# Performance work log

Hardware: AMD Instinct MI355X
Metric: run time of the kernel (lower is better)

Reference implementation:

```python
import jax, jax.numpy as jnp
import numpy as np

BATCH = 2048
INPUT_DIM = 256    # == output_units, since Dense output is fed back into the cell
DEC_UNITS = 1024
OUTPUT_STEPS = 96
OUTPUT_UNITS = 256


def setup_inputs() -> dict:
    key = jax.random.key(0)
    ks = jax.random.split(key, 8)
    scale = 0.05
    return {
        "last_input": jax.random.normal(ks[0], (BATCH, INPUT_DIM), dtype=jnp.float32),
        "h0": jax.random.normal(ks[1], (BATCH, DEC_UNITS), dtype=jnp.float32),
        "c0": jax.random.normal(ks[2], (BATCH, DEC_UNITS), dtype=jnp.float32),
        # LSTMCell params (Keras layout: kernel [in, 4*units], recurrent_kernel [units, 4*units], bias [4*units]; gate order i,f,c,o)
        "Wk": jax.random.normal(ks[3], (INPUT_DIM, 4 * DEC_UNITS), dtype=jnp.float32) * scale,
        "Wr": jax.random.normal(ks[4], (DEC_UNITS, 4 * DEC_UNITS), dtype=jnp.float32) * scale,
        "b": jax.random.normal(ks[5], (4 * DEC_UNITS,), dtype=jnp.float32) * scale,
        # Dense output projection
        "Wd": jax.random.normal(ks[6], (DEC_UNITS, OUTPUT_UNITS), dtype=jnp.float32) * scale,
        "bd": jax.random.normal(ks[7], (OUTPUT_UNITS,), dtype=jnp.float32) * scale,
    }


def reference(last_input, h0, c0, Wk, Wr, b, Wd, bd):
    def step(carry, _):
        x, h, c = carry
        # fused gate GEMM: [B, in] @ [in, 4U] + [B, U] @ [U, 4U]
        z = x @ Wk + h @ Wr + b
        zi, zf, zg, zo = jnp.split(z, 4, axis=-1)  # Keras gate order: i, f, c(g), o
        i = jax.nn.sigmoid(zi)
        f = jax.nn.sigmoid(zf)
        o = jax.nn.sigmoid(zo)
        c_new = f * c + i * jnp.tanh(zg)
        h_new = o * jnp.tanh(c_new)
        pred = h_new @ Wd + bd  # fed back as next step's input
        return (pred, h_new, c_new), pred

    _, preds = jax.lax.scan(step, (last_input, h0, c0), None, length=OUTPUT_STEPS)
    # preds: [T, B, out] -> [B, T, out] (matches tf.transpose(predictions, [1,0,2]))
    return jnp.transpose(preds, (1, 0, 2))
```

## Files before the change

kernel.cpp:

```cpp
#include <hip/hip_runtime.h>
#include <hip/hip_bf16.h>
#include <stdint.h>

#define B_SZ 2048
#define U_SZ 1024
#define G_SZ 4096
#define I_SZ 256
#define O_SZ 256
#define T_SZ 96
#define K1_SZ 1280

typedef _Float16 half8 __attribute__((ext_vector_type(8)));
typedef float float4v __attribute__((ext_vector_type(4)));

__device__ inline float sigm_f(float x) { return 1.0f / (1.0f + __expf(-x)); }
__device__ inline float tanh_f(float x) { return 1.0f - 2.0f / (1.0f + __expf(2.0f * x)); }

__device__ inline short f2h(float x) {
    return __builtin_bit_cast(short, (_Float16)x);
}

__device__ inline void cp16(const void* g, void* l) {
    __builtin_amdgcn_global_load_lds(
        (const __attribute__((address_space(1))) void*)g,
        (__attribute__((address_space(3))) void*)l,
        16, 0, 0);
}


__global__ void transpose_reord(const float* __restrict__ in, float* __restrict__ out, int K) {
    __shared__ float s[32][33];
    int c0 = blockIdx.x * 32, k0 = blockIdx.y * 32;
    int tx = threadIdx.x, ty = threadIdx.y;
#pragma unroll
    for (int i = 0; i < 4; i++)
        s[ty + 8 * i][tx] = in[(long)(k0 + ty + 8 * i) * G_SZ + c0 + tx];
    __syncthreads();
#pragma unroll
    for (int i = 0; i < 4; i++) {
        int cc = ty + 8 * i;
        int c = c0 + cc;
        int n = 4 * (c & 1023) + (c >> 10);
        out[(long)n * K + k0 + tx] = s[tx][cc];
    }
}

__global__ void transpose_f32(const float* __restrict__ in, float* __restrict__ out, int R, int C) {
    __shared__ float s[32][33];
    int c0 = blockIdx.x * 32, r0 = blockIdx.y * 32;
    int tx = threadIdx.x, ty = threadIdx.y;
#pragma unroll
    for (int i = 0; i < 4; i++)
        s[ty + 8 * i][tx] = in[(long)(r0 + ty + 8 * i) * C + c0 + tx];
    __syncthreads();
#pragma unroll
    for (int i = 0; i < 4; i++)
        out[(long)(c0 + ty + 8 * i) * R + r0 + tx] = s[tx][ty + 8 * i];
}

__global__ void transpose_f16(const float* __restrict__ in, short* __restrict__ out, int R, int C) {
    __shared__ float s[32][33];
    int c0 = blockIdx.x * 32, r0 = blockIdx.y * 32;
    int tx = threadIdx.x, ty = threadIdx.y;
#pragma unroll
    for (int i = 0; i < 4; i++)
        s[ty + 8 * i][tx] = in[(long)(r0 + ty + 8 * i) * C + c0 + tx];
    __syncthreads();
#pragma unroll
    for (int i = 0; i < 4; i++)
        out[(long)(c0 + ty + 8 * i) * R + r0 + tx] = f2h(s[tx][ty + 8 * i]);
}

__global__ void fold_gemm(const float* __restrict__ WkT, const float* __restrict__ WrT,
                          const float* __restrict__ Wd, short* __restrict__ WeT) {
    __shared__ float sA[16][17];
    __shared__ float sB[16][17];
    int tx = threadIdx.x, ty = threadIdx.y;
    int n0 = blockIdx.x * 16, k0 = blockIdx.y * 16;
    float acc = 0.0f;
    for (int pc = 0; pc < I_SZ; pc += 16) {
        sA[ty][tx] = WkT[(long)(n0 + ty) * I_SZ + pc + tx];
        sB[ty][tx] = Wd[(long)(k0 + ty) * I_SZ + pc + tx];
        __syncthreads();
#pragma unroll
        for (int x = 0; x < 16; x++) acc += sA[ty][x] * sB[tx][x];
        __syncthreads();
    }
    long n = n0 + ty, k = k0 + tx;
    WeT[n * U_SZ + k] = f2h(WrT[n * U_SZ + k] + acc);
}

__global__ void build_b0t(const float* __restrict__ WkT, const float* __restrict__ WrT,
                          short* __restrict__ B0T) {
    long idx = (long)blockIdx.x * 256 + threadIdx.x;
    long n = idx / K1_SZ, k = idx % K1_SZ;
    float v = (k < I_SZ) ? WkT[n * I_SZ + k] : WrT[n * U_SZ + (k - I_SZ)];
    B0T[idx] = f2h(v);
}

__global__ void build_x0(const float* __restrict__ x0, const float* __restrict__ h0,
                         short* __restrict__ X0) {
    long idx = (long)blockIdx.x * 256 + threadIdx.x;
    long m = idx / K1_SZ, k = idx % K1_SZ;
    float v = (k < I_SZ) ? x0[m * I_SZ + k] : h0[m * U_SZ + (k - I_SZ)];
    X0[idx] = f2h(v);
}

__global__ void build_ber(const float* __restrict__ Wk, const float* __restrict__ b,
                          const float* __restrict__ bd, float* __restrict__ beR,
                          float* __restrict__ bR) {
    int c = blockIdx.x * 256 + threadIdx.x;
    float s = 0.0f;
    for (int p = 0; p < I_SZ; p++) s += bd[p] * Wk[(long)p * G_SZ + c];
    int slot = 4 * (c & 1023) + (c >> 10);
    bR[slot] = b[c];
    beR[slot] = b[c] + s;
}

__global__ __launch_bounds__(256, 2) void lstm_step(
    const short* __restrict__ A, const short* __restrict__ Bm, int K,
    float* __restrict__ cT, const float* __restrict__ beR, short* __restrict__ hOut) {
    __shared__ char smem[65536];

    const int tid = threadIdx.x;
    const int w = tid >> 6, l = tid & 63;
    const int wg = w >> 1, wb = w & 1;
    const int n_blk = blockIdx.x, m_blk = blockIdx.y;
    const long Kb = (long)K * 2;

    float4v acc[4][4];
#pragma unroll
    for (int i = 0; i < 4; i++)
#pragma unroll
        for (int j = 0; j < 4; j++) acc[i][j] = (float4v)0.0f;

    const int r8 = l >> 3;
    const int s8 = l & 7;
    const int gch = s8 ^ r8;
    const char* gA = (const char*)A + ((long)(n_blk * 128 + w * 32 + r8)) * Kb + gch * 16;
    const char* gB = (const char*)Bm + ((long)(m_blk * 128 + w * 32 + r8)) * Kb + gch * 16;

    const int lr = l & 15;
    const int lk = l >> 4;

    auto stage = [&](int kt, int b) {
        const long go = (long)kt * 128;
        char* lA = smem + b * 32768 + (w * 32) * 128;
        char* lB = smem + b * 32768 + 16384 + (w * 32) * 128;
#pragma unroll
        for (int ci = 0; ci < 4; ++ci) {
            cp16(gA + (long)ci * 8 * Kb + go, lA + ci * 1024);
            cp16(gB + (long)ci * 8 * Kb + go, lB + ci * 1024);
        }
    };
    auto compute = [&](int b) {
        const char* As = smem + b * 32768;
        const char* Bs = smem + b * 32768 + 16384;
#pragma unroll
        for (int ks = 0; ks < 2; ++ks) {
            half8 af[4], bf[4];
            const int chunk = (ks * 4 + lk) ^ (lr & 7);
#pragma unroll
            for (int mi = 0; mi < 4; ++mi)
                af[mi] = *(const half8*)(As + (wg * 64 + mi * 16 + lr) * 128 + chunk * 16);
#pragma unroll
            for (int ni = 0; ni < 4; ++ni)
                bf[ni] = *(const half8*)(Bs + (wb * 64 + ni * 16 + lr) * 128 + chunk * 16);
#pragma unroll
            for (int mi = 0; mi < 4; ++mi)
#pragma unroll
                for (int ni = 0; ni < 4; ++ni)
                    acc[mi][ni] = __builtin_amdgcn_mfma_f32_16x16x32_f16(
                        af[mi], bf[ni], acc[mi][ni], 0, 0, 0);
        }
    };

    const int KI = K >> 6;
    stage(0, 0);
    for (int kt = 0; kt < KI; kt += 2) {
        __syncthreads();
        if (kt + 1 < KI) stage(kt + 1, 1);
        compute(0);
        __syncthreads();
        if (kt + 2 < KI) stage(kt + 2, 0);
        compute(1);
    }

    short* hs = (short*)smem;
    __syncthreads();
    const int j_base = n_blk * 32 + wg * 16;
    const int m_base = m_blk * 128 + wb * 64;
#pragma unroll
    for (int mi = 0; mi < 4; ++mi) {
        int j = j_base + mi * 4 + lk;
        float4v bias = *(const float4v*)(beR + 4 * j);
#pragma unroll
        for (int ni = 0; ni < 4; ++ni) {
            int m = m_base + ni * 16 + lr;
            float zi = acc[mi][ni][0] + bias[0];
            float zf = acc[mi][ni][1] + bias[1];
            float zg = acc[mi][ni][2] + bias[2];
            float zo = acc[mi][ni][3] + bias[3];
            float ig = sigm_f(zi), fg = sigm_f(zf), gg = tanh_f(zg), og = sigm_f(zo);
            long cidx = (long)j * B_SZ + m;
            float cn = fg * cT[cidx] + ig * gg;
            cT[cidx] = cn;
            float h = og * tanh_f(cn);
            hs[(wb * 64 + ni * 16 + lr) * 32 + (wg * 16 + mi * 4 + lk)] = f2h(h);
        }
    }
    __syncthreads();
    {
        int q = tid & 3;
        for (int rr = tid >> 2; rr < 128; rr += 64) {
            uint4 v = *(const uint4*)(hs + rr * 32 + q * 8);
            *(uint4*)(hOut + (long)(m_blk * 128 + rr) * U_SZ + n_blk * 32 + q * 8) = v;
        }
    }
}

__global__ __launch_bounds__(256, 2) void dense_out(
    const short* __restrict__ Hm, const short* __restrict__ WdT,
    const float* __restrict__ bd, float* __restrict__ out, int t_fix) {
    __shared__ char smem[65536];

    const int tid = threadIdx.x;
    const int w = tid >> 6, l = tid & 63;
    const int wg = w >> 1, wb = w & 1;
    const int m_blk = blockIdx.x, o_blk = blockIdx.y;
    const long Kb = U_SZ * 2;

    float4v acc[4][4];
#pragma unroll
    for (int i = 0; i < 4; i++)
#pragma unroll
        for (int j = 0; j < 4; j++) acc[i][j] = (float4v)0.0f;

    const int r8 = l >> 3;
    const int s8 = l & 7;
    const int gch = s8 ^ r8;
    const char* gA = (const char*)Hm + ((long)(m_blk * 128 + w * 32 + r8)) * Kb + gch * 16;
    const char* gB = (const char*)WdT + ((long)(o_blk * 128 + w * 32 + r8)) * Kb + gch * 16;

    const int lr = l & 15;
    const int lk = l >> 4;

    auto stage = [&](int kt, int b) {
        const long go = (long)kt * 128;
        char* lA = smem + b * 32768 + (w * 32) * 128;
        char* lB = smem + b * 32768 + 16384 + (w * 32) * 128;
#pragma unroll
        for (int ci = 0; ci < 4; ++ci) {
            cp16(gA + (long)ci * 8 * Kb + go, lA + ci * 1024);
            cp16(gB + (long)ci * 8 * Kb + go, lB + ci * 1024);
        }
    };
    auto compute = [&](int b) {
        const char* As = smem + b * 32768;
        const char* Bs = smem + b * 32768 + 16384;
#pragma unroll
        for (int ks = 0; ks < 2; ++ks) {
            half8 af[4], bf[4];
            const int chunk = (ks * 4 + lk) ^ (lr & 7);
#pragma unroll
            for (int mi = 0; mi < 4; ++mi)
                af[mi] = *(const half8*)(As + (wg * 64 + mi * 16 + lr) * 128 + chunk * 16);
#pragma unroll
            for (int ni = 0; ni < 4; ++ni)
                bf[ni] = *(const half8*)(Bs + (wb * 64 + ni * 16 + lr) * 128 + chunk * 16);
#pragma unroll
            for (int mi = 0; mi < 4; ++mi)
#pragma unroll
                for (int ni = 0; ni < 4; ++ni)
                    acc[mi][ni] = __builtin_amdgcn_mfma_f32_16x16x32_f16(
                        af[mi], bf[ni], acc[mi][ni], 0, 0, 0);
        }
    };

    const int KI = U_SZ >> 6;
    stage(0, 0);
    for (int kt = 0; kt < KI; kt += 2) {
        __syncthreads();
        if (kt + 1 < KI) stage(kt + 1, 1);
        compute(0);
        __syncthreads();
        if (kt + 2 < KI) stage(kt + 2, 0);
        compute(1);
    }

#pragma unroll
    for (int mi = 0; mi < 4; ++mi) {
#pragma unroll
        for (int ni = 0; ni < 4; ++ni) {
            int o = o_blk * 128 + wb * 64 + ni * 16 + lr;
            float bo = bd[o];
#pragma unroll
            for (int r = 0; r < 4; ++r) {
                int m = m_blk * 128 + wg * 64 + mi * 16 + lk * 4 + r;
                int t = (t_fix >= 0) ? t_fix : (m >> 11);
                int b = (t_fix >= 0) ? m : (m & 2047);
                out[(long)b * (T_SZ * O_SZ) + (long)t * O_SZ + o] = acc[mi][ni][r] + bo;
            }
        }
    }
}

extern "C" void kernel_launch(void* const* d_in, const int* in_sizes, int n_in,
                              void* d_out, int out_size, void* d_ws, size_t ws_size,
                              hipStream_t stream) {
    (void)in_sizes; (void)n_in; (void)out_size;
    const float* x0 = (const float*)d_in[0];
    const float* h0 = (const float*)d_in[1];
    const float* c0 = (const float*)d_in[2];
    const float* Wk = (const float*)d_in[3];
    const float* Wr = (const float*)d_in[4];
    const float* bb = (const float*)d_in[5];
    const float* Wd = (const float*)d_in[6];
    const float* bd = (const float*)d_in[7];
    float* out = (float*)d_out;

    char* p = (char*)d_ws;
    auto alloc = [&](size_t bytes) {
        char* r = p;
        p += (bytes + 255) & ~(size_t)255;
        return r;
    };
    short* WeT = (short*)alloc((size_t)G_SZ * U_SZ * 2);
    short* B0T = (short*)alloc((size_t)G_SZ * K1_SZ * 2);
    short* X0 = (short*)alloc((size_t)B_SZ * K1_SZ * 2);
    short* WdT = (short*)alloc((size_t)O_SZ * U_SZ * 2);
    float* beR = (float*)alloc((size_t)U_SZ * 4 * 4);
    float* bR = (float*)alloc((size_t)U_SZ * 4 * 4);
    float* cT = (float*)alloc((size_t)U_SZ * B_SZ * 4);
    char* R = p;
    const size_t SLAB = (size_t)B_SZ * U_SZ * 2;
    size_t rem = (ws_size > (size_t)(R - (char*)d_ws)) ? ws_size - (size_t)(R - (char*)d_ws) : 0;
    bool hist = rem >= (size_t)T_SZ * SLAB;

    float* WkT = (float*)R;
    float* WrT = (float*)(R + (size_t)G_SZ * I_SZ * 4);

    transpose_reord<<<dim3(G_SZ / 32, I_SZ / 32), dim3(32, 8), 0, stream>>>(Wk, WkT, I_SZ);
    transpose_reord<<<dim3(G_SZ / 32, U_SZ / 32), dim3(32, 8), 0, stream>>>(Wr, WrT, U_SZ);
    fold_gemm<<<dim3(G_SZ / 16, U_SZ / 16), dim3(16, 16), 0, stream>>>(WkT, WrT, Wd, WeT);
    build_b0t<<<(int)(((size_t)G_SZ * K1_SZ) / 256), 256, 0, stream>>>(WkT, WrT, B0T);
    build_ber<<<G_SZ / 256, 256, 0, stream>>>(Wk, bb, bd, beR, bR);
    transpose_f16<<<dim3(O_SZ / 32, U_SZ / 32), dim3(32, 8), 0, stream>>>(Wd, WdT, U_SZ, O_SZ);
    transpose_f32<<<dim3(U_SZ / 32, B_SZ / 32), dim3(32, 8), 0, stream>>>(c0, cT, B_SZ, U_SZ);
    build_x0<<<(int)(((size_t)B_SZ * K1_SZ) / 256), 256, 0, stream>>>(x0, h0, X0);

    auto slab = [&](int t) -> short* {
        if (hist) return (short*)(R + (size_t)(t - 1) * SLAB);
        return (short*)(R + (size_t)((t - 1) & 1) * SLAB);
    };

    for (int t = 1; t <= T_SZ; ++t) {
        if (t == 1)
            lstm_step<<<dim3(G_SZ / 128, B_SZ / 128), 256, 0, stream>>>(
                B0T, X0, K1_SZ, cT, bR, slab(1));
        else
            lstm_step<<<dim3(G_SZ / 128, B_SZ / 128), 256, 0, stream>>>(
                WeT, slab(t - 1), U_SZ, cT, beR, slab(t));
        if (!hist)
            dense_out<<<dim3(B_SZ / 128, 2), 256, 0, stream>>>(slab(t), WdT, bd, out, t - 1);
    }
    if (hist)
        dense_out<<<dim3((T_SZ * B_SZ) / 128, 2), 256, 0, stream>>>((short*)R, WdT, bd, out, -1);
}
```

Baseline: 2.903 ms.

## Use 256x128 tiles with a triple-buffered async pipeline and an MFMA weight fold

Factors the GEMM main loop into a shared core that uses 512-thread blocks with 256x128 output tiles. It triple-buffers the LDS stages, waiting with explicit vmcnt counts so one prefetch stays in flight, and raises wave priority around the MFMA bursts. The one-time weight-fold GEMM moves from a scalar shared-memory kernel to the MFMA core using fp16-cast inputs. The h staging buffer is XOR-swizzled to avoid bank conflicts. The change trades occupancy for reuse: 144KB of LDS per block likely allows only one block per CU, and the recurrent step grid shrinks to 256 blocks.

```diff
diff --git a/kernel.cpp b/kernel.cpp
--- a/kernel.cpp
+++ b/kernel.cpp
@@ -71,23 +71,9 @@
         out[(long)(c0 + ty + 8 * i) * R + r0 + tx] = f2h(s[tx][ty + 8 * i]);
 }
 
-__global__ void fold_gemm(const float* __restrict__ WkT, const float* __restrict__ WrT,
-                          const float* __restrict__ Wd, short* __restrict__ WeT) {
-    __shared__ float sA[16][17];
-    __shared__ float sB[16][17];
-    int tx = threadIdx.x, ty = threadIdx.y;
-    int n0 = blockIdx.x * 16, k0 = blockIdx.y * 16;
-    float acc = 0.0f;
-    for (int pc = 0; pc < I_SZ; pc += 16) {
-        sA[ty][tx] = WkT[(long)(n0 + ty) * I_SZ + pc + tx];
-        sB[ty][tx] = Wd[(long)(k0 + ty) * I_SZ + pc + tx];
-        __syncthreads();
-#pragma unroll
-        for (int x = 0; x < 16; x++) acc += sA[ty][x] * sB[tx][x];
-        __syncthreads();
-    }
-    long n = n0 + ty, k = k0 + tx;
-    WeT[n * U_SZ + k] = f2h(WrT[n * U_SZ + k] + acc);
+__global__ void cast_f16(const float* __restrict__ in, short* __restrict__ out) {
+    long i = (long)blockIdx.x * 256 + threadIdx.x;
+    out[i] = f2h(in[i]);
 }
 
 __global__ void build_b0t(const float* __restrict__ WkT, const float* __restrict__ WrT,
@@ -117,10 +103,68 @@
     beR[slot] = b[c] + s;
 }
 
-__global__ __launch_bounds__(256, 2) void lstm_step(
+__device__ __forceinline__ void gemm_core(char* smem, const char* gA, const char* gB,
+                                          long Kb, int KI, int w, int l,
+                                          float4v (&acc)[4][4]) {
+    const int lr = l & 15, lk = l >> 4;
+    const int wg = w >> 1, wb = w & 1;
+    char* const lA = smem + (w * 32) * 128;
+    char* const lB = smem + 32768 + (w * 16) * 128;
+
+    auto stage = [&](int kt, int b) {
+        const long go = (long)kt * 128;
+        char* dA = lA + b * 49152;
+        char* dB = lB + b * 49152;
+#pragma unroll
+        for (int ci = 0; ci < 4; ++ci) cp16(gA + (long)ci * 8 * Kb + go, dA + ci * 1024);
+#pragma unroll
+        for (int ci = 0; ci < 2; ++ci) cp16(gB + (long)ci * 8 * Kb + go, dB + ci * 1024);
+    };
+    auto compute = [&](int b) {
+        const char* As = smem + b * 49152;
+        const char* Bs = As + 32768;
+#pragma unroll
+        for (int ks = 0; ks < 2; ++ks) {
+            half8 af[4], bf[4];
+            const int chunk = (ks * 4 + lk) ^ (lr & 7);
+#pragma unroll
+            for (int mi = 0; mi < 4; ++mi)
+                af[mi] = *(const half8*)(As + (wg * 64 + mi * 16 + lr) * 128 + chunk * 16);
+#pragma unroll
+            for (int ni = 0; ni < 4; ++ni)
+                bf[ni] = *(const half8*)(Bs + (wb * 64 + ni * 16 + lr) * 128 + chunk * 16);
+            __builtin_amdgcn_s_setprio(1);
+#pragma unroll
+            for (int mi = 0; mi < 4; ++mi)
+#pragma unroll
+                for (int ni = 0; ni < 4; ++ni)
+                    acc[mi][ni] = __builtin_amdgcn_mfma_f32_16x16x32_f16(
+                        af[mi], bf[ni], acc[mi][ni], 0, 0, 0);
+            __builtin_amdgcn_s_setprio(0);
+        }
+    };
+
+    stage(0, 0);
+    stage(1, 1);
+    int bc = 0, bs = 2;
+    for (int kt = 0; kt < KI; ++kt) {
+        if (kt < KI - 1)
+            asm volatile("s_waitcnt vmcnt(6) lgkmcnt(0)" ::: "memory");
+        else
+            asm volatile("s_waitcnt vmcnt(0) lgkmcnt(0)" ::: "memory");
+        __builtin_amdgcn_s_barrier();
+        asm volatile("" ::: "memory");
+        if (kt + 2 < KI) stage(kt + 2, bs);
+        compute(bc);
+        bc = (bc == 2) ? 0 : bc + 1;
+        bs = (bs == 2) ? 0 : bs + 1;
+    }
+}
+
+__global__ __launch_bounds__(512, 2) void lstm_step(
     const short* __restrict__ A, const short* __restrict__ Bm, int K,
     float* __restrict__ cT, const float* __restrict__ beR, short* __restrict__ hOut) {
-    __shared__ char smem[65536];
+    __shared__ char smem[147456];
 
     const int tid = threadIdx.x;
     const int w = tid >> 6, l = tid & 63;
@@ -137,58 +181,15 @@
     const int r8 = l >> 3;
     const int s8 = l & 7;
     const int gch = s8 ^ r8;
-    const char* gA = (const char*)A + ((long)(n_blk * 128 + w * 32 + r8)) * Kb + gch * 16;
-    const char* gB = (const char*)Bm + ((long)(m_blk * 128 + w * 32 + r8)) * Kb + gch * 16;
-
-    const int lr = l & 15;
-    const int lk = l >> 4;
-
-    auto stage = [&](int kt, int b) {
-        const long go = (long)kt * 128;
-        char* lA = smem + b * 32768 + (w * 32) * 128;
-        char* lB = smem + b * 32768 + 16384 + (w * 32) * 128;
-#pragma unroll
-        for (int ci = 0; ci < 4; ++ci) {
-            cp16(gA + (long)ci * 8 * Kb + go, lA + ci * 1024);
-            cp16(gB + (long)ci * 8 * Kb + go, lB + ci * 1024);
-        }
-    };
-    auto compute = [&](int b) {
-        const char* As = smem + b * 32768;
-        const char* Bs = smem + b * 32768 + 16384;
-#pragma unroll
-        for (int ks = 0; ks < 2; ++ks) {
-            half8 af[4], bf[4];
-            const int chunk = (ks * 4 + lk) ^ (lr & 7);
-#pragma unroll
-            for (int mi = 0; mi < 4; ++mi)
-                af[mi] = *(const half8*)(As + (wg * 64 + mi * 16 + lr) * 128 + chunk * 16);
-#pragma unroll
-            for (int ni = 0; ni < 4; ++ni)
-                bf[ni] = *(const half8*)(Bs + (wb * 64 + ni * 16 + lr) * 128 + chunk * 16);
-#pragma unroll
-            for (int mi = 0; mi < 4; ++mi)
-#pragma unroll
-                for (int ni = 0; ni < 4; ++ni)
-                    acc[mi][ni] = __builtin_amdgcn_mfma_f32_16x16x32_f16(
-                        af[mi], bf[ni], acc[mi][ni], 0, 0, 0);
-        }
-    };
-
-    const int KI = K >> 6;
-    stage(0, 0);
-    for (int kt = 0; kt < KI; kt += 2) {
-        __syncthreads();
-        if (kt + 1 < KI) stage(kt + 1, 1);
-        compute(0);
-        __syncthreads();
-        if (kt + 2 < KI) stage(kt + 2, 0);
-        compute(1);
-    }
-
+    const char* gA = (const char*)A + ((long)(n_blk * 256 + w * 32 + r8)) * Kb + gch * 16;
+    const char* gB = (const char*)Bm + ((long)(m_blk * 128 + w * 16 + r8)) * Kb + gch * 16;
+
+    gemm_core(smem, gA, gB, Kb, K >> 6, w, l, acc);
+
+    const int lr = l & 15, lk = l >> 4;
     short* hs = (short*)smem;
     __syncthreads();
-    const int j_base = n_blk * 32 + wg * 16;
+    const int j_base = n_blk * 64 + wg * 16;
     const int m_base = m_blk * 128 + wb * 64;
 #pragma unroll
     for (int mi = 0; mi < 4; ++mi) {
@@ -206,28 +207,32 @@
             float cn = fg * cT[cidx] + ig * gg;
             cT[cidx] = cn;
             float h = og * tanh_f(cn);
-            hs[(wb * 64 + ni * 16 + lr) * 32 + (wg * 16 + mi * 4 + lk)] = f2h(h);
+            int mm = wb * 64 + ni * 16 + lr;
+            int jj = wg * 16 + mi * 4 + lk;
+            hs[mm * 64 + (jj ^ ((mm & 7) << 3))] = f2h(h);
         }
     }
     __syncthreads();
     {
-        int q = tid & 3;
-        for (int rr = tid >> 2; rr < 128; rr += 64) {
-            uint4 v = *(const uint4*)(hs + rr * 32 + q * 8);
-            *(uint4*)(hOut + (long)(m_blk * 128 + rr) * U_SZ + n_blk * 32 + q * 8) = v;
+        const int q = tid & 7;
+        int rr = tid >> 3;
+#pragma unroll
+        for (int it = 0; it < 2; ++it, rr += 64) {
+            uint4 v = *(const uint4*)(hs + rr * 64 + ((q ^ (rr & 7)) * 8));
+            *(uint4*)(hOut + (long)(m_blk * 128 + rr) * U_SZ + n_blk * 64 + q * 8) = v;
         }
     }
 }
 
-__global__ __launch_bounds__(256, 2) void dense_out(
+__global__ __launch_bounds__(512, 2) void dense_out(
     const short* __restrict__ Hm, const short* __restrict__ WdT,
     const float* __restrict__ bd, float* __restrict__ out, int t_fix) {
-    __shared__ char smem[65536];
+    __shared__ char smem[147456];
 
     const int tid = threadIdx.x;
     const int w = tid >> 6, l = tid & 63;
     const int wg = w >> 1, wb = w & 1;
-    const int m_blk = blockIdx.x, o_blk = blockIdx.y;
+    const int o_blk = blockIdx.x, m_blk = blockIdx.y;
     const long Kb = U_SZ * 2;
 
     float4v acc[4][4];
@@ -236,73 +241,64 @@
 #pragma unroll
         for (int j = 0; j < 4; j++) acc[i][j] = (float4v)0.0f;
 
-    const int r8 = l >> 3;
-    const int s8 = l & 7;
-    const int gch = s8 ^ r8;
-    const char* gA = (const char*)Hm + ((long)(m_blk * 128 + w * 32 + r8)) * Kb + gch * 16;
-    const char* gB = (const char*)WdT + ((long)(o_blk * 128 + w * 32 + r8)) * Kb + gch * 16;
-
-    const int lr = l & 15;
-    const int lk = l >> 4;
-
-    auto stage = [&](int kt, int b) {
-        const long go = (long)kt * 128;
-        char* lA = smem + b * 32768 + (w * 32) * 128;
-        char* lB = smem + b * 32768 + 16384 + (w * 32) * 128;
-#pragma unroll
-        for (int ci = 0; ci < 4; ++ci) {
-            cp16(gA + (long)ci * 8 * Kb + go, lA + ci * 1024);
-            cp16(gB + (long)ci * 8 * Kb + go, lB + ci * 1024);
-        }
-    };
-    auto compute = [&](int b) {
-        const char* As = smem + b * 32768;
-        const char* Bs = smem + b * 32768 + 16384;
-#pragma unroll
-        for (int ks = 0; ks < 2; ++ks) {
-            half8 af[4], bf[4];
-            const int chunk = (ks * 4 + lk) ^ (lr & 7);
-#pragma unroll
-            for (int mi = 0; mi < 4; ++mi)
-                af[mi] = *(const half8*)(As + (wg * 64 + mi * 16 + lr) * 128 + chunk * 16);
-#pragma unroll
-            for (int ni = 0; ni < 4; ++ni)
-                bf[ni] = *(const half8*)(Bs + (wb * 64 + ni * 16 + lr) * 128 + chunk * 16);
-#pragma unroll
-            for (int mi = 0; mi < 4; ++mi)
-#pragma unroll
-                for (int ni = 0; ni < 4; ++ni)
-                    acc[mi][ni] = __builtin_amdgcn_mfma_f32_16x16x32_f16(
-                        af[mi], bf[ni], acc[mi][ni], 0, 0, 0);
-        }
-    };
-
-    const int KI = U_SZ >> 6;
-    stage(0, 0);
-    for (int kt = 0; kt < KI; kt += 2) {
-        __syncthreads();
-        if (kt + 1 < KI) stage(kt + 1, 1);
-        compute(0);
-        __syncthreads();
-        if (kt + 2 < KI) stage(kt + 2, 0);
-        compute(1);
-    }
-
-#pragma unroll
-    for (int mi = 0; mi < 4; ++mi) {
-#pragma unroll
-        for (int ni = 0; ni < 4; ++ni) {
-            int o = o_blk * 128 + wb * 64 + ni * 16 + lr;
-            float bo = bd[o];
+    const int r8 = l >> 3, s8 = l & 7, gch = s8 ^ r8;
+    const char* gA = (const char*)Hm + ((long)(m_blk * 256 + w * 32 + r8)) * Kb + gch * 16;
+    const char* gB = (const char*)WdT + ((long)(o_blk * 128 + w * 16 + r8)) * Kb + gch * 16;
+
+    gemm_core(smem, gA, gB, Kb, U_SZ >> 6, w, l, acc);
+
+    const int lr = l & 15, lk = l >> 4;
+#pragma unroll
+    for (int ni = 0; ni < 4; ++ni) {
+        int o = o_blk * 128 + wb * 64 + ni * 16 + lr;
+        float bo = bd[o];
+#pragma unroll
+        for (int mi = 0; mi < 4; ++mi) {
 #pragma unroll
             for (int r = 0; r < 4; ++r) {
-                int m = m_blk * 128 + wg * 64 + mi * 16 + lk * 4 + r;
+                int m = m_blk * 256 + wg * 64 + mi * 16 + lk * 4 + r;
                 int t = (t_fix >= 0) ? t_fix : (m >> 11);
                 int b = (t_fix >= 0) ? m : (m & 2047);
                 out[(long)b * (T_SZ * O_SZ) + (long)t * O_SZ + o] = acc[mi][ni][r] + bo;
             }
         }
     }
+}
+
+__global__ __launch_bounds__(512, 2) void fold_mfma(
+    const short* __restrict__ WkTh, const short* __restrict__ Wdh,
+    const float* __restrict__ WrT, short* __restrict__ WeT) {
+    __shared__ char smem[147456];
+
+    const int tid = threadIdx.x;
+    const int w = tid >> 6, l = tid & 63;
+    const int wg = w >> 1, wb = w & 1;
+    const int n_blk = blockIdx.x, k_blk = blockIdx.y;
+    const long Kb = I_SZ * 2;
+
+    float4v acc[4][4];
+#pragma unroll
+    for (int i = 0; i < 4; i++)
+#pragma unroll
+        for (int j = 0; j < 4; j++) acc[i][j] = (float4v)0.0f;
+
+    const int r8 = l >> 3, s8 = l & 7, gch = s8 ^ r8;
+    const char* gA = (const char*)WkTh + ((long)(n_blk * 256 + w * 32 + r8)) * Kb + gch * 16;
+    const char* gB = (const char*)Wdh + ((long)(k_blk * 128 + w * 16 + r8)) * Kb + gch * 16;
+
+    gemm_core(smem, gA, gB, Kb, I_SZ >> 6, w, l, acc);
+
+    const int lr = l & 15, lk = l >> 4;
+#pragma unroll
+    for (int mi = 0; mi < 4; ++mi)
+#pragma unroll
+        for (int ni = 0; ni < 4; ++ni)
+#pragma unroll
+            for (int r = 0; r < 4; ++r) {
+                long n = n_blk * 256 + wg * 64 + mi * 16 + lk * 4 + r;
+                long k = k_blk * 128 + wb * 64 + ni * 16 + lr;
+                WeT[n * U_SZ + k] = f2h(WrT[n * U_SZ + k] + acc[mi][ni][r]);
+            }
 }
 
 extern "C" void kernel_launch(void* const* d_in, const int* in_sizes, int n_in,
@@ -329,6 +325,8 @@
     short* B0T = (short*)alloc((size_t)G_SZ * K1_SZ * 2);
     short* X0 = (short*)alloc((size_t)B_SZ * K1_SZ * 2);
     short* WdT = (short*)alloc((size_t)O_SZ * U_SZ * 2);
+    short* WkTh = (short*)alloc((size_t)G_SZ * I_SZ * 2);
+    short* Wdh = (short*)alloc((size_t)U_SZ * I_SZ * 2);
     float* beR = (float*)alloc((size_t)U_SZ * 4 * 4);
     float* bR = (float*)alloc((size_t)U_SZ * 4 * 4);
     float* cT = (float*)alloc((size_t)U_SZ * B_SZ * 4);
@@ -342,7 +340,9 @@
 
     transpose_reord<<<dim3(G_SZ / 32, I_SZ / 32), dim3(32, 8), 0, stream>>>(Wk, WkT, I_SZ);
     transpose_reord<<<dim3(G_SZ / 32, U_SZ / 32), dim3(32, 8), 0, stream>>>(Wr, WrT, U_SZ);
-    fold_gemm<<<dim3(G_SZ / 16, U_SZ / 16), dim3(16, 16), 0, stream>>>(WkT, WrT, Wd, WeT);
+    cast_f16<<<(G_SZ * I_SZ) / 256, 256, 0, stream>>>(WkT, WkTh);
+    cast_f16<<<(U_SZ * I_SZ) / 256, 256, 0, stream>>>(Wd, Wdh);
+    fold_mfma<<<dim3(G_SZ / 256, U_SZ / 128), 512, 0, stream>>>(WkTh, Wdh, WrT, WeT);
     build_b0t<<<(int)(((size_t)G_SZ * K1_SZ) / 256), 256, 0, stream>>>(WkT, WrT, B0T);
     build_ber<<<G_SZ / 256, 256, 0, stream>>>(Wk, bb, bd, beR, bR);
     transpose_f16<<<dim3(O_SZ / 32, U_SZ / 32), dim3(32, 8), 0, stream>>>(Wd, WdT, U_SZ, O_SZ);
@@ -356,14 +356,14 @@
 
     for (int t = 1; t <= T_SZ; ++t) {
         if (t == 1)
-            lstm_step<<<dim3(G_SZ / 128, B_SZ / 128), 256, 0, stream>>>(
+            lstm_step<<<dim3(G_SZ / 256, B_SZ / 128), 512, 0, stream>>>(
                 B0T, X0, K1_SZ, cT, bR, slab(1));
         else
-            lstm_step<<<dim3(G_SZ / 128, B_SZ / 128), 256, 0, stream>>>(
+            lstm_step<<<dim3(G_SZ / 256, B_SZ / 128), 512, 0, stream>>>(
                 WeT, slab(t - 1), U_SZ, cT, beR, slab(t));
         if (!hist)
-            dense_out<<<dim3(B_SZ / 128, 2), 256, 0, stream>>>(slab(t), WdT, bd, out, t - 1);
+            dense_out<<<dim3(2, B_SZ / 256), 512, 0, stream>>>(slab(t), WdT, bd, out, t - 1);
     }
     if (hist)
-        dense_out<<<dim3((T_SZ * B_SZ) / 128, 2), 256, 0, stream>>>((short*)R, WdT, bd, out, -1);
-}
+        dense_out<<<dim3(2, (T_SZ * B_SZ) / 256), 512, 0, stream>>>((short*)R, WdT, bd, out, -1);
+}
```

Result: faster. 2.737 ms (-5.7%).
